# Kernel optimization log

Hardware: AMD Instinct MI355X
Metric: run time of the kernel (lower is better)

The kernel has to match this reference:

```python
import jax, jax.numpy as jnp
import numpy as np

B, N, E, D, H, HW, L = 16, 32, 256, 256, 8, 784, 4
DH = D // H
FF = 4 * D
BN = B * N
BE = B * E
SCALE = 1.0 / np.sqrt(DH)


def _ln(x, g, b):
    m = x.mean(-1, keepdims=True)
    v = ((x - m) ** 2).mean(-1, keepdims=True)
    return (x - m) * jax.lax.rsqrt(v + 1e-5) * g + b


def setup_inputs() -> dict:
    key = jax.random.key(0)
    ks = iter(jax.random.split(key, 64))
    def w(shape, s=0.05):
        return jax.random.normal(next(ks), shape, jnp.float32) * s
    inp = {
        'nodes': w((B, N, D), 1.0),
        'edges': w((B, E, D), 1.0),
        'images': w((B, HW, D), 1.0),
        'mask': jnp.zeros((B * H, N + E, HW), jnp.float32),
        'node_enc': w((BN, D), 1.0),
        'edge_enc': w((BE, D), 1.0),
        'ln1_g': jnp.ones((L, D), jnp.float32), 'ln1_b': jnp.zeros((L, D), jnp.float32),
        'Wqkv': w((L, D, 3 * D)), 'bqkv': jnp.zeros((L, 3 * D), jnp.float32),
        'Wo': w((L, D, D)), 'bo': jnp.zeros((L, D), jnp.float32),
        'ls1': jnp.full((L, D), 0.1, jnp.float32),
        'ln2_g': jnp.ones((L, D), jnp.float32), 'ln2_b': jnp.zeros((L, D), jnp.float32),
        'Wn1': w((L, D, D)), 'bn1': jnp.zeros((L, D), jnp.float32),
        'Wn2': w((L, D, D)), 'bn2': jnp.zeros((L, D), jnp.float32),
        'We': w((L, D, D)), 'be': jnp.zeros((L, D), jnp.float32),
        'attn_p': w((L, H, DH), 1.0),
        'Weo': w((L, D, D)), 'beo': jnp.zeros((L, D), jnp.float32),
        'Wno': w((L, D, D)), 'bno': jnp.zeros((L, D), jnp.float32),
        'ls2': jnp.full((L, D), 0.1, jnp.float32),
        'ln3_g': jnp.ones((L, D), jnp.float32), 'ln3_b': jnp.zeros((L, D), jnp.float32),
        'W1': w((L, D, FF)), 'b1': jnp.zeros((L, FF), jnp.float32),
        'W2': w((L, FF, D)), 'b2': jnp.zeros((L, D), jnp.float32),
        'ls3': jnp.full((L, D), 0.1, jnp.float32),
        'edge_index': jax.random.randint(next(ks), (2, BE), 0, BN, jnp.int32),
    }
    return inp


def reference(nodes, edges, images, mask, node_enc, edge_enc,
              ln1_g, ln1_b, Wqkv, bqkv, Wo, bo, ls1,
              ln2_g, ln2_b, Wn1, bn1, Wn2, bn2, We, be, attn_p, Weo, beo, Wno, bno, ls2,
              ln3_g, ln3_b, W1, b1, W2, b2, ls3, edge_index):
    idx0, idx1 = edge_index[0], edge_index[1]
    ne = jnp.concatenate([nodes, edges], axis=1)  # [B, N+E, D]
    mask4 = mask.reshape(B, H, N + E, HW)
    for l in range(L):
        # cross-attention ne -> images
        ne1n = _ln(ne, ln1_g[l], ln1_b[l])
        q = (ne1n @ Wqkv[l, :, :D] + bqkv[l, :D]).reshape(B, N + E, H, DH)
        k = (images @ Wqkv[l, :, D:2 * D] + bqkv[l, D:2 * D]).reshape(B, HW, H, DH)
        v = (images @ Wqkv[l, :, 2 * D:] + bqkv[l, 2 * D:]).reshape(B, HW, H, DH)
        scores = jnp.einsum('bqhd,bkhd->bhqk', q, k) * SCALE + mask4
        attn = jax.nn.softmax(scores, axis=-1)
        ctx = jnp.einsum('bhqk,bkhd->bqhd', attn, v).reshape(B, N + E, D)
        ne1 = ne + ls1[l] * (ctx @ Wo[l] + bo[l])
        # modified GAT on flattened graph
        ne2n = _ln(ne1, ln2_g[l], ln2_b[l])
        nodes_f = ne2n[:, :N].reshape(BN, D) + node_enc
        edges_f = ne2n[:, N:].reshape(BE, D) + edge_enc
        fn = (nodes_f @ Wn1[l] + bn1[l])[idx0]
        sn = (nodes_f @ Wn2[l] + bn2[l])[idx0]  # NOTE: original code uses edge_index[0] here too
        ep = edges_f @ We[l] + be[l]
        hidden = jax.nn.gelu(fn + sn + ep, approximate=False)  # [BE, D]
        pres = (hidden.reshape(BE, H, DH) * attn_p[l]).sum(-1)  # [BE, H]
        mseg = jax.ops.segment_max(pres, idx0, num_segments=BN)
        expv = jnp.exp(pres - mseg[idx0])
        denom = jax.ops.segment_sum(expv, idx0, num_segments=BN)
        alpha = expv / denom[idx0]  # scatter_softmax over destination nodes
        new_edges = hidden @ Weo[l] + beo[l]
        vals = (nodes_f[idx1] + new_edges) @ Wno[l] + bno[l]
        vals = vals.reshape(BE, H, DH) * alpha[..., None]
        new_nodes = jax.ops.segment_sum(vals.reshape(BE, D), idx0, num_segments=BN)
        gat = jnp.concatenate([new_nodes.reshape(B, N, D), new_edges.reshape(B, E, D)], axis=1)
        ne2 = ne1 + ls2[l] * gat
        # FFN
        ne3n = _ln(ne2, ln3_g[l], ln3_b[l])
        ffn = jax.nn.gelu(ne3n @ W1[l] + b1[l], approximate=False) @ W2[l] + b2[l]
        ne = ne2 + ls3[l] * ffn
    return ne
```

## Files before the change

kernel.cpp:

```cpp
#include <hip/hip_runtime.h>
#include <math.h>

static constexpr int B_  = 16;
static constexpr int N_  = 32;
static constexpr int E_  = 256;
static constexpr int D_  = 256;
static constexpr int H_  = 8;
static constexpr int HW_ = 784;
static constexpr int L_  = 4;
static constexpr int DH_ = 32;
static constexpr int FF_ = 1024;
static constexpr int BN_ = 512;
static constexpr int BE_ = 4096;
static constexpr int NE_ = 288;
#define SCALE_ 0.17677669529663687f

static constexpr size_t LAYER_W = 1114112;
static constexpr size_t OFF_Q   = 0;
static constexpr size_t OFF_K   = 65536;
static constexpr size_t OFF_WO  = 196608;
static constexpr size_t OFF_WN1 = 262144;
static constexpr size_t OFF_WE  = 393216;
static constexpr size_t OFF_WEO = 458752;
static constexpr size_t OFF_WNO = 524288;
static constexpr size_t OFF_W1  = 589824;
static constexpr size_t OFF_W2  = 851968;

typedef __attribute__((ext_vector_type(8))) short bf16x8;
typedef __attribute__((ext_vector_type(4))) float f32x4;

__device__ __forceinline__ float gelu_f(float x) {
    return 0.5f * x * (1.0f + erff(x * 0.7071067811865476f));
}

__device__ __forceinline__ unsigned short f2bf(float x) {
    unsigned u = __float_as_uint(x);
    u += 0x7FFFu + ((u >> 16) & 1u);
    return (unsigned short)(u >> 16);
}
__device__ __forceinline__ unsigned pack2bf(float a, float b) {
    return (unsigned)f2bf(a) | ((unsigned)f2bf(b) << 16);
}
__device__ __forceinline__ float bf2f(unsigned short u) {
    return __uint_as_float(((unsigned)u) << 16);
}


__global__ void concat_kernel(const float* __restrict__ nodes, const float* __restrict__ edges,
                              float* __restrict__ ne) {
    int tid = blockIdx.x * 256 + threadIdx.x;
    int d = tid & 255;
    int row = tid >> 8;
    int b = row / NE_, pos = row % NE_;
    float v = (pos < N_) ? nodes[(size_t)(b * N_ + pos) * D_ + d]
                         : edges[(size_t)(b * E_ + (pos - N_)) * D_ + d];
    ne[tid] = v;
}

__global__ void imgcast_kernel(const float* __restrict__ img, unsigned short* __restrict__ out) {
    int tid = blockIdx.x * 256 + threadIdx.x;
    const float* p = img + (size_t)tid * 8;
    float4 a = *(const float4*)(p);
    float4 b = *(const float4*)(p + 4);
    uint4 o = make_uint4(pack2bf(a.x, a.y), pack2bf(a.z, a.w),
                         pack2bf(b.x, b.y), pack2bf(b.z, b.w));
    *(uint4*)&out[(size_t)tid * 8] = o;
}

__device__ __forceinline__ float ln_from_val(float v, int d,
                                             const float* __restrict__ g, const float* __restrict__ bta,
                                             float* sh1, float* sh2) {
    float s = v, s2 = v * v;
    #pragma unroll
    for (int o = 32; o >= 1; o >>= 1) { s += __shfl_down(s, o); s2 += __shfl_down(s2, o); }
    int lane = d & 63, w = d >> 6;
    if (lane == 0) { sh1[w] = s; sh2[w] = s2; }
    __syncthreads();
    if (d == 0) {
        float a = sh1[0] + sh1[1] + sh1[2] + sh1[3];
        float c = sh2[0] + sh2[1] + sh2[2] + sh2[3];
        sh1[0] = a; sh2[0] = c;
    }
    __syncthreads();
    float mean = sh1[0] * (1.0f / D_);
    float var  = sh2[0] * (1.0f / D_) - mean * mean;
    float rstd = rsqrtf(var + 1e-5f);
    return (v - mean) * rstd * g[d] + bta[d];
}

__global__ __launch_bounds__(256) void ln_kernel(const float* __restrict__ x,
                                                 unsigned short* __restrict__ y,
                                                 const float* __restrict__ g,
                                                 const float* __restrict__ bta) {
    __shared__ float sh1[4], sh2[4];
    const int row = blockIdx.x, d = threadIdx.x;
    float v = x[(size_t)row * D_ + d];
    y[(size_t)row * D_ + d] = f2bf(ln_from_val(v, d, g, bta, sh1, sh2));
}

__global__ __launch_bounds__(256) void ln2enc_kernel(const float* __restrict__ x,
                                                     const float* __restrict__ g,
                                                     const float* __restrict__ bta,
                                                     const float* __restrict__ node_enc,
                                                     const float* __restrict__ edge_enc,
                                                     unsigned short* __restrict__ nodes_f,
                                                     unsigned short* __restrict__ edges_f) {
    __shared__ float sh1[4], sh2[4];
    const int row = blockIdx.x, d = threadIdx.x;
    float v = x[(size_t)row * D_ + d];
    float val = ln_from_val(v, d, g, bta, sh1, sh2);
    int b = row / NE_, pos = row % NE_;
    if (pos < N_) {
        int rn = b * N_ + pos;
        nodes_f[(size_t)rn * D_ + d] = f2bf(val + node_enc[(size_t)rn * D_ + d]);
    } else {
        int re = b * E_ + (pos - N_);
        edges_f[(size_t)re * D_ + d] = f2bf(val + edge_enc[(size_t)re * D_ + d]);
    }
}

__global__ __launch_bounds__(256) void gatres_ln_kernel(
    float* __restrict__ ne, const float* __restrict__ new_nodes,
    const float* __restrict__ new_edges, const float* __restrict__ ls2l,
    const float* __restrict__ g, const float* __restrict__ bta,
    unsigned short* __restrict__ lnb) {
    __shared__ float sh1[4], sh2[4];
    const int row = blockIdx.x, d = threadIdx.x;
    int b = row / NE_, pos = row % NE_;
    float gv = (pos < N_) ? new_nodes[(size_t)(b * N_ + pos) * D_ + d]
                          : new_edges[(size_t)(b * E_ + (pos - N_)) * D_ + d];
    float v = ne[(size_t)row * D_ + d] + ls2l[d] * gv;
    ne[(size_t)row * D_ + d] = v;
    lnb[(size_t)row * D_ + d] = f2bf(ln_from_val(v, d, g, bta, sh1, sh2));
}

__global__ __launch_bounds__(256) void wtrans_kernel(
    const float* __restrict__ Wqkv, const float* __restrict__ Wo,
    const float* __restrict__ Wn1,  const float* __restrict__ Wn2,
    const float* __restrict__ We,   const float* __restrict__ Weo,
    const float* __restrict__ Wno,  const float* __restrict__ W1,
    const float* __restrict__ W2,   unsigned short* __restrict__ wT)
{
    const int bid = blockIdx.x;
    const int l = bid / 1088;
    int tl = bid % 1088;
    const float* src; int ld, K, Nn; unsigned short* dst;
    if (tl < 576) {
        int mid = tl >> 6; tl &= 63;
        K = 256; Nn = 256;
        if (mid < 3) {
            src = Wqkv + (size_t)l * 256 * 768 + mid * 256; ld = 768;
            dst = wT + (size_t)l * LAYER_W + (size_t)mid * 65536;
        } else {
            const float* bases[6] = {Wo, Wn1, Wn2, We, Weo, Wno};
            src = bases[mid - 3] + (size_t)l * 65536; ld = 256;
            dst = wT + (size_t)l * LAYER_W + OFF_WO + (size_t)(mid - 3) * 65536;
        }
    } else if (tl < 832) {
        tl -= 576; K = 256; Nn = 1024;
        src = W1 + (size_t)l * 262144; ld = 1024;
        dst = wT + (size_t)l * LAYER_W + OFF_W1;
    } else {
        tl -= 832; K = 1024; Nn = 256;
        src = W2 + (size_t)l * 262144; ld = 256;
        dst = wT + (size_t)l * LAYER_W + OFF_W2;
    }
    const int ntn = Nn >> 5;
    const int k0 = (tl / ntn) << 5, n0 = (tl % ntn) << 5;
    __shared__ float ts[32][33];
    const int t = threadIdx.x;
    const int kl = t >> 5, nl = t & 31;
    #pragma unroll
    for (int rr = 0; rr < 4; ++rr)
        ts[kl + rr * 8][nl] = src[(size_t)(k0 + kl + rr * 8) * ld + n0 + nl];
    __syncthreads();
    const int onl = t >> 3, okl = (t & 7) << 2;
    ushort4 o;
    o.x = f2bf(ts[okl + 0][onl]); o.y = f2bf(ts[okl + 1][onl]);
    o.z = f2bf(ts[okl + 2][onl]); o.w = f2bf(ts[okl + 3][onl]);
    *(ushort4*)&dst[(size_t)(n0 + onl) * K + k0 + okl] = o;
}

template<int MODE, int OUTBF>
__global__ __launch_bounds__(256) void mgemm_kernel(
    const unsigned short* __restrict__ A, int lda,
    const unsigned short* __restrict__ Bt,
    const float* __restrict__ bias,
    const float* __restrict__ bias2,
    const float* __restrict__ res,
    const float* __restrict__ ls,
    void* __restrict__ Cv, int ldc, int K)
{
    __shared__ unsigned short As[64][72];
    __shared__ unsigned short Bs[64][72];
    const int m0 = blockIdx.y * 64, n0 = blockIdx.x * 64;
    const int t = threadIdx.x;
    const int l = t & 63, w = t >> 6;
    const int wr = (w >> 1) * 32, wc = (w & 1) * 32;
    const int srow = t >> 2, skc = (t & 3) * 16;
    const int frow = l & 15, kg = l >> 4;
    f32x4 acc[2][2];
    acc[0][0] = (f32x4){0.f,0.f,0.f,0.f}; acc[0][1] = acc[0][0];
    acc[1][0] = acc[0][0];                acc[1][1] = acc[0][0];
    for (int k0 = 0; k0 < K; k0 += 64) {
        const unsigned short* ap = A + (size_t)(m0 + srow) * lda + k0 + skc;
        uint4 aq0 = *(const uint4*)(ap);
        uint4 aq1 = *(const uint4*)(ap + 8);
        const unsigned short* bp = Bt + (size_t)(n0 + srow) * K + k0 + skc;
        uint4 bq0 = *(const uint4*)(bp);
        uint4 bq1 = *(const uint4*)(bp + 8);
        __syncthreads();
        *(uint4*)&As[srow][skc]     = aq0;
        *(uint4*)&As[srow][skc + 8] = aq1;
        *(uint4*)&Bs[srow][skc]     = bq0;
        *(uint4*)&Bs[srow][skc + 8] = bq1;
        __syncthreads();
        #pragma unroll
        for (int kk = 0; kk < 2; ++kk) {
            bf16x8 af0 = *(const bf16x8*)&As[wr + frow][kk * 32 + kg * 8];
            bf16x8 af1 = *(const bf16x8*)&As[wr + 16 + frow][kk * 32 + kg * 8];
            bf16x8 bf0 = *(const bf16x8*)&Bs[wc + frow][kk * 32 + kg * 8];
            bf16x8 bf1 = *(const bf16x8*)&Bs[wc + 16 + frow][kk * 32 + kg * 8];
            acc[0][0] = __builtin_amdgcn_mfma_f32_16x16x32_bf16(af0, bf0, acc[0][0], 0, 0, 0);
            acc[0][1] = __builtin_amdgcn_mfma_f32_16x16x32_bf16(af0, bf1, acc[0][1], 0, 0, 0);
            acc[1][0] = __builtin_amdgcn_mfma_f32_16x16x32_bf16(af1, bf0, acc[1][0], 0, 0, 0);
            acc[1][1] = __builtin_amdgcn_mfma_f32_16x16x32_bf16(af1, bf1, acc[1][1], 0, 0, 0);
        }
    }
    #pragma unroll
    for (int fr = 0; fr < 2; ++fr) {
        #pragma unroll
        for (int fc = 0; fc < 2; ++fc) {
            int n = n0 + wc + fc * 16 + frow;
            float bv = (bias2 != nullptr && n >= 256) ? bias2[n - 256] : bias[n];
            float lv = (MODE == 2) ? ls[n] : 0.f;
            #pragma unroll
            for (int rg = 0; rg < 4; ++rg) {
                int m = m0 + wr + fr * 16 + kg * 4 + rg;
                float vv = acc[fr][fc][rg] + bv;
                if (MODE == 1) vv = gelu_f(vv);
                if (MODE == 2) vv = res[(size_t)m * ldc + n] + lv * vv;
                if (OUTBF) ((unsigned short*)Cv)[(size_t)m * ldc + n] = f2bf(vv);
                else       ((float*)Cv)[(size_t)m * ldc + n] = vv;
            }
        }
    }
}

__global__ __launch_bounds__(128) void attn_kernel(
    const unsigned short* __restrict__ q, const unsigned short* __restrict__ kv,
    const float* __restrict__ mask, unsigned short* __restrict__ ctx)
{
    const int bid = blockIdx.x;
    const int h = bid & 7;
    const int qt = (bid >> 3) % 9;
    const int b = (bid >> 3) / 9;
    const int q0 = qt * 32;
    const int t = threadIdx.x;
    const int w = t >> 6, l = t & 63;
    const int lr = l & 15, lg = l >> 4;
    constexpr int NC = (HW_ + 63) / 64;

    __shared__ unsigned short Ks[2][64][40];
    __shared__ unsigned short Vs[2][32][72];
    __shared__ unsigned short Pl[2][16][72];
    __shared__ unsigned short Msk[2][32][68];

    bf16x8 qfrag = *(const bf16x8*)(q + ((size_t)(b * NE_ + q0 + w * 16 + lr)) * D_ + h * DH_ + lg * 8);

    const int kkey = t >> 1, kdh = (t & 1) * 16;
    const int vdh = (t & 7) * 4, vk0 = (t >> 3) * 2;
    const int mrow = t >> 2, mcg = (t & 3) * 16;
    const unsigned short* kbase = kv + ((size_t)b * HW_) * 512 + h * DH_;
    const unsigned short* vbase = kv + ((size_t)b * HW_) * 512 + 256 + h * DH_;
    const float* mbase = mask + ((size_t)(b * H_ + h) * NE_ + q0 + mrow) * (size_t)HW_;

    uint4 kq0, kq1;
    ushort4 va[2], vb4[2];
    float mf[16];

    auto issue_kv = [&](int c0) {
        {
            int key = c0 + kkey;
            bool ok = key < HW_;
            const unsigned short* kp = kbase + (size_t)(ok ? key : 0) * 512 + kdh;
            kq0 = *(const uint4*)(kp);
            kq1 = *(const uint4*)(kp + 8);
            if (!ok) { kq0 = make_uint4(0,0,0,0); kq1 = kq0; }
        }
        #pragma unroll
        for (int r = 0; r < 2; ++r) {
            int key = c0 + vk0 + 32 * r;
            bool ok0 = key < HW_, ok1 = (key + 1) < HW_;
            const unsigned short* vp = vbase + (size_t)(ok0 ? key : 0) * 512 + vdh;
            va[r]  = *(const ushort4*)(vp);
            vb4[r] = *(const ushort4*)(vp + (ok1 ? 512 : 0));
            if (!ok0) va[r]  = make_ushort4(0,0,0,0);
            if (!ok1) vb4[r] = make_ushort4(0,0,0,0);
        }
    };
    auto issue_mask = [&](int c0) {
        if (c0 + 64 <= HW_) {
            #pragma unroll
            for (int i = 0; i < 4; ++i) {
                float4 m4 = *(const float4*)(mbase + c0 + mcg + i * 4);
                mf[i * 4 + 0] = m4.x; mf[i * 4 + 1] = m4.y;
                mf[i * 4 + 2] = m4.z; mf[i * 4 + 3] = m4.w;
            }
        } else {
            #pragma unroll
            for (int i = 0; i < 16; ++i) {
                int col = c0 + mcg + i;
                mf[i] = (col < HW_) ? mbase[col] : -1e30f;
            }
        }
    };
    auto write_kv = [&](int bufi) {
        *(uint4*)&Ks[bufi][kkey][kdh]     = kq0;
        *(uint4*)&Ks[bufi][kkey][kdh + 8] = kq1;
        #pragma unroll
        for (int r = 0; r < 2; ++r) {
            const unsigned short* a = (const unsigned short*)&va[r];
            const unsigned short* c = (const unsigned short*)&vb4[r];
            #pragma unroll
            for (int i = 0; i < 4; ++i)
                *(unsigned*)&Vs[bufi][vdh + i][vk0 + 32 * r] = (unsigned)a[i] | ((unsigned)c[i] << 16);
        }
    };
    auto write_mask = [&](int bufi) {
        uint4 p0 = make_uint4(pack2bf(mf[0], mf[1]),  pack2bf(mf[2], mf[3]),
                              pack2bf(mf[4], mf[5]),  pack2bf(mf[6], mf[7]));
        uint4 p1 = make_uint4(pack2bf(mf[8], mf[9]),  pack2bf(mf[10], mf[11]),
                              pack2bf(mf[12], mf[13]), pack2bf(mf[14], mf[15]));
        *(uint4*)&Msk[bufi][mrow][mcg]     = p0;
        *(uint4*)&Msk[bufi][mrow][mcg + 8] = p1;
    };

    f32x4 oacc[2];
    oacc[0] = (f32x4){0.f, 0.f, 0.f, 0.f}; oacc[1] = oacc[0];
    float m_i[4] = {-INFINITY, -INFINITY, -INFINITY, -INFINITY};
    float l_i[4] = {0.f, 0.f, 0.f, 0.f};

    issue_kv(0);
    issue_mask(0);
    write_kv(0);
    write_mask(0);
    __syncthreads();

    for (int c = 0; c < NC; ++c) {
        const int c0 = c * 64;
        const int cb = c & 1, nb = cb ^ 1;
        if (c + 1 < NC) { issue_kv(c0 + 64); issue_mask(c0 + 64); }

        f32x4 sacc[4];
        #pragma unroll
        for (int fc = 0; fc < 4; ++fc) {
            sacc[fc] = (f32x4){0.f, 0.f, 0.f, 0.f};
            bf16x8 kf = *(const bf16x8*)&Ks[cb][fc * 16 + lr][lg * 8];
            sacc[fc] = __builtin_amdgcn_mfma_f32_16x16x32_bf16(qfrag, kf, sacc[fc], 0, 0, 0);
        }
        float s[4][4];
        #pragma unroll
        for (int fc = 0; fc < 4; ++fc)
            #pragma unroll
            for (int rg = 0; rg < 4; ++rg)
                s[fc][rg] = sacc[fc][rg] * SCALE_ + bf2f(Msk[cb][w * 16 + lg * 4 + rg][fc * 16 + lr]);

        float mloc[4];
        #pragma unroll
        for (int rg = 0; rg < 4; ++rg)
            mloc[rg] = fmaxf(fmaxf(s[0][rg], s[1][rg]), fmaxf(s[2][rg], s[3][rg]));
        #pragma unroll
        for (int off = 1; off < 16; off <<= 1)
            #pragma unroll
            for (int rg = 0; rg < 4; ++rg)
                mloc[rg] = fmaxf(mloc[rg], __shfl_xor(mloc[rg], off));
        float scl[4], lloc[4];
        #pragma unroll
        for (int rg = 0; rg < 4; ++rg) {
            float mn = fmaxf(m_i[rg], mloc[rg]);
            scl[rg] = __expf(m_i[rg] - mn);
            m_i[rg] = mn;
        }
        #pragma unroll
        for (int rg = 0; rg < 4; ++rg) {
            float acc = 0.f;
            #pragma unroll
            for (int fc = 0; fc < 4; ++fc) {
                float p = __expf(s[fc][rg] - m_i[rg]);
                s[fc][rg] = p;
                acc += p;
            }
            lloc[rg] = acc;
        }
        #pragma unroll
        for (int off = 1; off < 16; off <<= 1)
            #pragma unroll
            for (int rg = 0; rg < 4; ++rg)
                lloc[rg] += __shfl_xor(lloc[rg], off);
        #pragma unroll
        for (int rg = 0; rg < 4; ++rg) {
            l_i[rg] = l_i[rg] * scl[rg] + lloc[rg];
            oacc[0][rg] *= scl[rg];
            oacc[1][rg] *= scl[rg];
        }

        #pragma unroll
        for (int fc = 0; fc < 4; ++fc)
            #pragma unroll
            for (int rg = 0; rg < 4; ++rg)
                Pl[w][lg * 4 + rg][fc * 16 + lr] = f2bf(s[fc][rg]);
        #pragma unroll
        for (int ks2 = 0; ks2 < 2; ++ks2) {
            bf16x8 pf = *(const bf16x8*)&Pl[w][lr][ks2 * 32 + lg * 8];
            #pragma unroll
            for (int d2 = 0; d2 < 2; ++d2) {
                bf16x8 vf = *(const bf16x8*)&Vs[cb][d2 * 16 + lr][ks2 * 32 + lg * 8];
                oacc[d2] = __builtin_amdgcn_mfma_f32_16x16x32_bf16(pf, vf, oacc[d2], 0, 0, 0);
            }
        }

        if (c + 1 < NC) {
            write_kv(nb);
            write_mask(nb);
            __syncthreads();
        }
    }

    unsigned short* cbase = ctx + ((size_t)(b * NE_ + q0 + w * 16 + lg * 4)) * D_ + h * DH_;
    #pragma unroll
    for (int rg = 0; rg < 4; ++rg) {
        float inv = 1.0f / l_i[rg];
        #pragma unroll
        for (int d2 = 0; d2 < 2; ++d2)
            cbase[(size_t)rg * D_ + d2 * 16 + lr] = f2bf(oacc[d2][rg] * inv);
    }
}


__global__ __launch_bounds__(256) void hidden_kernel(
    const float* __restrict__ gn12,
    unsigned short* __restrict__ hid, const int* __restrict__ idx0,
    const float* __restrict__ attn_p_l, float* __restrict__ pres) {
    int e = blockIdx.x;
    int d = threadIdx.x;
    int n = idx0[e];
    float x = bf2f(hid[(size_t)e * D_ + d]) + gn12[(size_t)n * 512 + d] + gn12[(size_t)n * 512 + 256 + d];
    float hv = gelu_f(x);
    hid[(size_t)e * D_ + d] = f2bf(hv);
    float pr = hv * attn_p_l[d];
    #pragma unroll
    for (int o = 1; o < 32; o <<= 1) pr += __shfl_xor(pr, o);
    if ((d & 31) == 0) pres[e * H_ + (d >> 5)] = pr;
}

__global__ void segsoft_kernel(const float* __restrict__ pres, const int* __restrict__ csr_off,
                               const int* __restrict__ csr_perm,
                               float* __restrict__ mseg, float* __restrict__ denom) {
    int tid = blockIdx.x * 256 + threadIdx.x;
    int n = tid >> 3, h = tid & 7;
    int s = csr_off[n], e2 = csr_off[n + 1];
    float mx = -INFINITY;
    for (int i = s; i < e2; ++i) mx = fmaxf(mx, pres[csr_perm[i] * H_ + h]);
    float sum = 0.f;
    for (int i = s; i < e2; ++i) sum += expf(pres[csr_perm[i] * H_ + h] - mx);
    mseg[tid] = mx;
    denom[tid] = sum;
}

__global__ void vin_kernel(const unsigned short* __restrict__ nodes_f,
                           const float* __restrict__ new_edges,
                           const int* __restrict__ idx1, unsigned short* __restrict__ vin) {
    int tid = blockIdx.x * 256 + threadIdx.x;
    int e = tid >> 8, d = tid & 255;
    vin[tid] = f2bf(bf2f(nodes_f[(size_t)idx1[e] * D_ + d]) + new_edges[tid]);
}

__global__ __launch_bounds__(256) void nodeagg_kernel(
    const float* __restrict__ vals, const float* __restrict__ pres,
    const float* __restrict__ mseg, const float* __restrict__ denom,
    const int* __restrict__ csr_off, const int* __restrict__ csr_perm,
    float* __restrict__ new_nodes) {
    int n = blockIdx.x;
    int d = threadIdx.x;
    int s = csr_off[n], e2 = csr_off[n + 1];
    int h = d >> 5;
    float ms = mseg[n * H_ + h];
    float rd = 1.0f / denom[n * H_ + h];
    float acc = 0.f;
    for (int i = s; i < e2; ++i) {
        int e = csr_perm[i];
        float a = expf(pres[e * H_ + h] - ms) * rd;
        acc += vals[(size_t)e * D_ + d] * a;
    }
    new_nodes[(size_t)n * D_ + d] = acc;
}


__global__ void zero_counts(int* counts) {
    int t = blockIdx.x * 256 + threadIdx.x;
    if (t < BN_) counts[t] = 0;
}

__global__ void csr_count(const int* __restrict__ idx0, int* __restrict__ counts) {
    int e = blockIdx.x * 256 + threadIdx.x;
    if (e < BE_) atomicAdd(&counts[idx0[e]], 1);
}

__global__ __launch_bounds__(512) void csr_scan(const int* __restrict__ counts, int* __restrict__ csr_off) {
    __shared__ int buf[BN_];
    int t = threadIdx.x;
    int c = counts[t];
    buf[t] = c;
    __syncthreads();
    for (int o = 1; o < BN_; o <<= 1) {
        int add = (t >= o) ? buf[t - o] : 0;
        __syncthreads();
        buf[t] += add;
        __syncthreads();
    }
    csr_off[t] = buf[t] - c;
    if (t == BN_ - 1) csr_off[BN_] = buf[t];
}

__global__ __launch_bounds__(64) void csr_fill(const int* __restrict__ idx0,
                                               const int* __restrict__ csr_off,
                                               int* __restrict__ csr_perm) {
    int n = blockIdx.x;
    int lane = threadIdx.x;
    int w = csr_off[n];
    for (int c0 = 0; c0 < BE_; c0 += 64) {
        int e = c0 + lane;
        bool m = (idx0[e] == n);
        unsigned long long bal = __ballot(m);
        if (m) {
            int pre = __popcll(bal & ((1ull << lane) - 1ull));
            csr_perm[w + pre] = e;
        }
        w += __popcll(bal);
    }
}


static void launch_mgemm(hipStream_t s, int mode, int outbf,
                         const unsigned short* A, int lda, const unsigned short* Bt,
                         const float* bias, const float* bias2, const float* res, const float* ls,
                         void* C, int ldc, int M, int N, int K) {
    dim3 g(N / 64, M / 64);
    if (mode == 0) {
        if (outbf) mgemm_kernel<0,1><<<g, 256, 0, s>>>(A, lda, Bt, bias, bias2, res, ls, C, ldc, K);
        else       mgemm_kernel<0,0><<<g, 256, 0, s>>>(A, lda, Bt, bias, bias2, res, ls, C, ldc, K);
    } else if (mode == 1) {
        mgemm_kernel<1,1><<<g, 256, 0, s>>>(A, lda, Bt, bias, bias2, res, ls, C, ldc, K);
    } else {
        mgemm_kernel<2,0><<<g, 256, 0, s>>>(A, lda, Bt, bias, bias2, res, ls, C, ldc, K);
    }
}

extern "C" void kernel_launch(void* const* d_in, const int* in_sizes, int n_in,
                              void* d_out, int out_size, void* d_ws, size_t ws_size,
                              hipStream_t stream) {
    const float* nodes    = (const float*)d_in[0];
    const float* edges    = (const float*)d_in[1];
    const float* images   = (const float*)d_in[2];
    const float* mask     = (const float*)d_in[3];
    const float* node_enc = (const float*)d_in[4];
    const float* edge_enc = (const float*)d_in[5];
    const float* ln1_g = (const float*)d_in[6];
    const float* ln1_b = (const float*)d_in[7];
    const float* Wqkv  = (const float*)d_in[8];
    const float* bqkv  = (const float*)d_in[9];
    const float* Wo    = (const float*)d_in[10];
    const float* bo    = (const float*)d_in[11];
    const float* ls1   = (const float*)d_in[12];
    const float* ln2_g = (const float*)d_in[13];
    const float* ln2_b = (const float*)d_in[14];
    const float* Wn1   = (const float*)d_in[15];
    const float* bn1   = (const float*)d_in[16];
    const float* Wn2   = (const float*)d_in[17];
    const float* bn2   = (const float*)d_in[18];
    const float* We    = (const float*)d_in[19];
    const float* be    = (const float*)d_in[20];
    const float* attn_p= (const float*)d_in[21];
    const float* Weo   = (const float*)d_in[22];
    const float* beo   = (const float*)d_in[23];
    const float* Wno   = (const float*)d_in[24];
    const float* bno   = (const float*)d_in[25];
    const float* ls2   = (const float*)d_in[26];
    const float* ln3_g = (const float*)d_in[27];
    const float* ln3_b = (const float*)d_in[28];
    const float* W1    = (const float*)d_in[29];
    const float* b1    = (const float*)d_in[30];
    const float* W2    = (const float*)d_in[31];
    const float* b2    = (const float*)d_in[32];
    const float* ls3   = (const float*)d_in[33];
    const int*   edge_index = (const int*)d_in[34];
    const int* idx0 = edge_index;
    const int* idx1 = edge_index + BE_;

    float* ne = (float*)d_out;

    float* cur = (float*)d_ws;
    auto alloc = [&](size_t nfl) { float* p = cur; cur += nfl; return p; };
    auto allocbf = [&](size_t nbf) { float* p = cur; cur += (nbf + 1) / 2; return (unsigned short*)p; };

    unsigned short* lnbuf   = allocbf((size_t)B_ * NE_ * D_);
    unsigned short* qb      = allocbf((size_t)B_ * NE_ * D_);
    unsigned short* kvb     = allocbf((size_t)B_ * HW_ * 512);
    unsigned short* ffnh    = kvb;
    unsigned short* imgbf   = allocbf((size_t)B_ * HW_ * D_);
    unsigned short* ctxb    = allocbf((size_t)B_ * NE_ * D_);
    unsigned short* nodes_f = allocbf((size_t)BN_ * D_);
    unsigned short* edges_f = allocbf((size_t)BE_ * D_);
    unsigned short* hid     = allocbf((size_t)BE_ * D_);
    unsigned short* vin     = allocbf((size_t)BE_ * D_);
    float* gn12     = alloc((size_t)BN_ * 512);
    float* pres     = alloc((size_t)BE_ * H_);
    float* mseg     = alloc((size_t)BN_ * H_);
    float* denom    = alloc((size_t)BN_ * H_);
    float* new_edges= alloc((size_t)BE_ * D_);
    float* valsb    = alloc((size_t)BE_ * D_);
    float* new_nodes= alloc((size_t)BN_ * D_);
    int* counts   = (int*)cur; cur += BN_;
    int* csr_off  = (int*)cur; cur += BN_ + 4;
    int* csr_perm = (int*)cur; cur += BE_;
    cur = (float*)(((uintptr_t)cur + 255) & ~(uintptr_t)255);
    unsigned short* wT = (unsigned short*)cur;

    wtrans_kernel<<<4 * 1088, 256, 0, stream>>>(Wqkv, Wo, Wn1, Wn2, We, Weo, Wno, W1, W2, wT);
    imgcast_kernel<<<(B_ * HW_ * D_) / (256 * 8), 256, 0, stream>>>(images, imgbf);
    zero_counts<<<2, 256, 0, stream>>>(counts);
    csr_count<<<BE_ / 256, 256, 0, stream>>>(idx0, counts);
    csr_scan<<<1, 512, 0, stream>>>(counts, csr_off);
    csr_fill<<<BN_, 64, 0, stream>>>(idx0, csr_off, csr_perm);
    concat_kernel<<<(B_ * NE_ * D_) / 256, 256, 0, stream>>>(nodes, edges, ne);

    for (int l = 0; l < L_; ++l) {
        const unsigned short* wTl = wT + (size_t)l * LAYER_W;
        const float* bqkv_l = bqkv + (size_t)l * 3 * D_;

        ln_kernel<<<B_ * NE_, 256, 0, stream>>>(ne, lnbuf, ln1_g + l * D_, ln1_b + l * D_);
        launch_mgemm(stream, 0, 1, lnbuf, D_, wTl + OFF_Q, bqkv_l, nullptr, nullptr, nullptr,
                     qb, D_, B_ * NE_, D_, D_);
        launch_mgemm(stream, 0, 1, imgbf, D_, wTl + OFF_K, bqkv_l + D_, nullptr, nullptr, nullptr,
                     kvb, 512, B_ * HW_, 512, D_);
        attn_kernel<<<1152, 128, 0, stream>>>(qb, kvb, mask, ctxb);
        launch_mgemm(stream, 2, 0, ctxb, D_, wTl + OFF_WO, bo + l * D_, nullptr, ne, ls1 + l * D_,
                     ne, D_, B_ * NE_, D_, D_);

        ln2enc_kernel<<<B_ * NE_, 256, 0, stream>>>(ne, ln2_g + l * D_, ln2_b + l * D_,
                                                    node_enc, edge_enc, nodes_f, edges_f);
        launch_mgemm(stream, 0, 0, nodes_f, D_, wTl + OFF_WN1, bn1 + l * D_, bn2 + l * D_,
                     nullptr, nullptr, gn12, 512, BN_, 512, D_);
        launch_mgemm(stream, 0, 1, edges_f, D_, wTl + OFF_WE, be + l * D_, nullptr, nullptr, nullptr,
                     hid, D_, BE_, D_, D_);
        hidden_kernel<<<BE_, 256, 0, stream>>>(gn12, hid, idx0, attn_p + (size_t)l * H_ * DH_, pres);
        segsoft_kernel<<<(BN_ * H_) / 256, 256, 0, stream>>>(pres, csr_off, csr_perm, mseg, denom);
        launch_mgemm(stream, 0, 0, hid, D_, wTl + OFF_WEO, beo + l * D_, nullptr, nullptr, nullptr,
                     new_edges, D_, BE_, D_, D_);
        vin_kernel<<<(BE_ * D_) / 256, 256, 0, stream>>>(nodes_f, new_edges, idx1, vin);
        launch_mgemm(stream, 0, 0, vin, D_, wTl + OFF_WNO, bno + l * D_, nullptr, nullptr, nullptr,
                     valsb, D_, BE_, D_, D_);
        nodeagg_kernel<<<BN_, 256, 0, stream>>>(valsb, pres, mseg, denom, csr_off, csr_perm, new_nodes);
        gatres_ln_kernel<<<B_ * NE_, 256, 0, stream>>>(ne, new_nodes, new_edges, ls2 + l * D_,
                                                       ln3_g + l * D_, ln3_b + l * D_, lnbuf);

        launch_mgemm(stream, 1, 1, lnbuf, D_, wTl + OFF_W1, b1 + l * FF_, nullptr, nullptr, nullptr,
                     ffnh, FF_, B_ * NE_, FF_, D_);
        launch_mgemm(stream, 2, 0, ffnh, FF_, wTl + OFF_W2, b2 + l * D_, nullptr, ne, ls3 + l * D_,
                     ne, D_, B_ * NE_, D_, FF_);
    }
}
```

Baseline: 675.8 us.

## Split attention over key halves with combine pass; use direct-to-LDS loads in GEMM

Result: slower. 704.4 us (+4.2%).

```diff
diff --git a/kernel.cpp b/kernel.cpp
--- a/kernel.cpp
+++ b/kernel.cpp
@@ -13,6 +13,7 @@
 static constexpr int BN_ = 512;
 static constexpr int BE_ = 4096;
 static constexpr int NE_ = 288;
+static constexpr int ROWS_ = B_ * H_ * NE_;
 #define SCALE_ 0.17677669529663687f
 
 static constexpr size_t LAYER_W = 1114112;
@@ -28,6 +29,13 @@
 
 typedef __attribute__((ext_vector_type(8))) short bf16x8;
 typedef __attribute__((ext_vector_type(4))) float f32x4;
+
+typedef __attribute__((address_space(1))) const unsigned int gas_uint;
+typedef __attribute__((address_space(3))) unsigned int las_uint;
+
+__device__ __forceinline__ void gload16(const unsigned short* g, unsigned short* lds) {
+    __builtin_amdgcn_global_load_lds((gas_uint*)g, (las_uint*)lds, 16, 0, 0);
+}
 
 __device__ __forceinline__ float gelu_f(float x) {
     return 0.5f * x * (1.0f + erff(x * 0.7071067811865476f));
@@ -191,41 +199,41 @@
     const float* __restrict__ ls,
     void* __restrict__ Cv, int ldc, int K)
 {
-    __shared__ unsigned short As[64][72];
-    __shared__ unsigned short Bs[64][72];
+    __shared__ __align__(16) unsigned short As[64 * 64];
+    __shared__ __align__(16) unsigned short Bs[64 * 64];
     const int m0 = blockIdx.y * 64, n0 = blockIdx.x * 64;
     const int t = threadIdx.x;
     const int l = t & 63, w = t >> 6;
     const int wr = (w >> 1) * 32, wc = (w & 1) * 32;
-    const int srow = t >> 2, skc = (t & 3) * 16;
     const int frow = l & 15, kg = l >> 4;
+    const int srow = w * 8 + (l >> 3);
+    const int scolh = 8 * ((l & 7) ^ (l >> 3));
+    const int ldsoff = w * 512;
+    const int sw = (frow & 7) << 3;
     f32x4 acc[2][2];
     acc[0][0] = (f32x4){0.f,0.f,0.f,0.f}; acc[0][1] = acc[0][0];
     acc[1][0] = acc[0][0];                acc[1][1] = acc[0][0];
     for (int k0 = 0; k0 < K; k0 += 64) {
-        const unsigned short* ap = A + (size_t)(m0 + srow) * lda + k0 + skc;
-        uint4 aq0 = *(const uint4*)(ap);
-        uint4 aq1 = *(const uint4*)(ap + 8);
-        const unsigned short* bp = Bt + (size_t)(n0 + srow) * K + k0 + skc;
-        uint4 bq0 = *(const uint4*)(bp);
-        uint4 bq1 = *(const uint4*)(bp + 8);
+        const unsigned short* ga = A  + (size_t)(m0 + srow) * lda + k0 + scolh;
+        const unsigned short* gb = Bt + (size_t)(n0 + srow) * K   + k0 + scolh;
+        gload16(ga,                As + ldsoff);
+        gload16(ga + 32 * lda,     As + ldsoff + 2048);
+        gload16(gb,                Bs + ldsoff);
+        gload16(gb + (size_t)32 * K, Bs + ldsoff + 2048);
         __syncthreads();
-        *(uint4*)&As[srow][skc]     = aq0;
-        *(uint4*)&As[srow][skc + 8] = aq1;
-        *(uint4*)&Bs[srow][skc]     = bq0;
-        *(uint4*)&Bs[srow][skc + 8] = bq1;
-        __syncthreads();
         #pragma unroll
         for (int kk = 0; kk < 2; ++kk) {
-            bf16x8 af0 = *(const bf16x8*)&As[wr + frow][kk * 32 + kg * 8];
-            bf16x8 af1 = *(const bf16x8*)&As[wr + 16 + frow][kk * 32 + kg * 8];
-            bf16x8 bf0 = *(const bf16x8*)&Bs[wc + frow][kk * 32 + kg * 8];
-            bf16x8 bf1 = *(const bf16x8*)&Bs[wc + 16 + frow][kk * 32 + kg * 8];
+            const int off = (kk * 32 + kg * 8) ^ sw;
+            bf16x8 af0 = *(const bf16x8*)&As[(wr + frow) * 64 + off];
+            bf16x8 af1 = *(const bf16x8*)&As[(wr + 16 + frow) * 64 + off];
+            bf16x8 bf0 = *(const bf16x8*)&Bs[(wc + frow) * 64 + off];
+            bf16x8 bf1 = *(const bf16x8*)&Bs[(wc + 16 + frow) * 64 + off];
             acc[0][0] = __builtin_amdgcn_mfma_f32_16x16x32_bf16(af0, bf0, acc[0][0], 0, 0, 0);
             acc[0][1] = __builtin_amdgcn_mfma_f32_16x16x32_bf16(af0, bf1, acc[0][1], 0, 0, 0);
             acc[1][0] = __builtin_amdgcn_mfma_f32_16x16x32_bf16(af1, bf0, acc[1][0], 0, 0, 0);
             acc[1][1] = __builtin_amdgcn_mfma_f32_16x16x32_bf16(af1, bf1, acc[1][1], 0, 0, 0);
         }
+        __syncthreads();
     }
     #pragma unroll
     for (int fr = 0; fr < 2; ++fr) {
@@ -247,37 +255,38 @@
     }
 }
 
-__global__ __launch_bounds__(128) void attn_kernel(
+__global__ __launch_bounds__(128) void attn_part_kernel(
     const unsigned short* __restrict__ q, const unsigned short* __restrict__ kv,
-    const float* __restrict__ mask, unsigned short* __restrict__ ctx)
+    const float* __restrict__ mask,
+    float* __restrict__ pm, float* __restrict__ pl, float* __restrict__ pO)
 {
     const int bid = blockIdx.x;
-    const int h = bid & 7;
-    const int qt = (bid >> 3) % 9;
-    const int b = (bid >> 3) / 9;
+    const int half = bid & 1;
+    const int h = (bid >> 1) & 7;
+    const int qt = (bid >> 4) % 9;
+    const int b = (bid >> 4) / 9;
     const int q0 = qt * 32;
     const int t = threadIdx.x;
     const int w = t >> 6, l = t & 63;
     const int lr = l & 15, lg = l >> 4;
-    constexpr int NC = (HW_ + 63) / 64;
+    const int cs = half ? 6 : 0;
+    const int nc = half ? 7 : 6;
 
     __shared__ unsigned short Ks[2][64][40];
     __shared__ unsigned short Vs[2][32][72];
     __shared__ unsigned short Pl[2][16][72];
-    __shared__ unsigned short Msk[2][32][68];
 
     bf16x8 qfrag = *(const bf16x8*)(q + ((size_t)(b * NE_ + q0 + w * 16 + lr)) * D_ + h * DH_ + lg * 8);
 
     const int kkey = t >> 1, kdh = (t & 1) * 16;
     const int vdh = (t & 7) * 4, vk0 = (t >> 3) * 2;
-    const int mrow = t >> 2, mcg = (t & 3) * 16;
     const unsigned short* kbase = kv + ((size_t)b * HW_) * 512 + h * DH_;
     const unsigned short* vbase = kv + ((size_t)b * HW_) * 512 + 256 + h * DH_;
-    const float* mbase = mask + ((size_t)(b * H_ + h) * NE_ + q0 + mrow) * (size_t)HW_;
+    const float* mbase = mask + ((size_t)(b * H_ + h) * NE_ + q0 + w * 16 + lg * 4) * (size_t)HW_;
 
     uint4 kq0, kq1;
     ushort4 va[2], vb4[2];
-    float mf[16];
+    float mreg[2][4][4];
 
     auto issue_kv = [&](int c0) {
         {
@@ -299,22 +308,6 @@
             if (!ok1) vb4[r] = make_ushort4(0,0,0,0);
         }
     };
-    auto issue_mask = [&](int c0) {
-        if (c0 + 64 <= HW_) {
-            #pragma unroll
-            for (int i = 0; i < 4; ++i) {
-                float4 m4 = *(const float4*)(mbase + c0 + mcg + i * 4);
-                mf[i * 4 + 0] = m4.x; mf[i * 4 + 1] = m4.y;
-                mf[i * 4 + 2] = m4.z; mf[i * 4 + 3] = m4.w;
-            }
-        } else {
-            #pragma unroll
-            for (int i = 0; i < 16; ++i) {
-                int col = c0 + mcg + i;
-                mf[i] = (col < HW_) ? mbase[col] : -1e30f;
-            }
-        }
-    };
     auto write_kv = [&](int bufi) {
         *(uint4*)&Ks[bufi][kkey][kdh]     = kq0;
         *(uint4*)&Ks[bufi][kkey][kdh + 8] = kq1;
@@ -327,13 +320,14 @@
                 *(unsigned*)&Vs[bufi][vdh + i][vk0 + 32 * r] = (unsigned)a[i] | ((unsigned)c[i] << 16);
         }
     };
-    auto write_mask = [&](int bufi) {
-        uint4 p0 = make_uint4(pack2bf(mf[0], mf[1]),  pack2bf(mf[2], mf[3]),
-                              pack2bf(mf[4], mf[5]),  pack2bf(mf[6], mf[7]));
-        uint4 p1 = make_uint4(pack2bf(mf[8], mf[9]),  pack2bf(mf[10], mf[11]),
-                              pack2bf(mf[12], mf[13]), pack2bf(mf[14], mf[15]));
-        *(uint4*)&Msk[bufi][mrow][mcg]     = p0;
-        *(uint4*)&Msk[bufi][mrow][mcg + 8] = p1;
+    auto issue_mask = [&](int c0, int set) {
+        #pragma unroll
+        for (int rg = 0; rg < 4; ++rg)
+            #pragma unroll
+            for (int fc = 0; fc < 4; ++fc) {
+                int col = c0 + fc * 16 + lr;
+                mreg[set][rg][fc] = (col < HW_) ? mbase[(size_t)rg * HW_ + col] : -1e30f;
+            }
     };
 
     f32x4 oacc[2];
@@ -341,16 +335,17 @@
     float m_i[4] = {-INFINITY, -INFINITY, -INFINITY, -INFINITY};
     float l_i[4] = {0.f, 0.f, 0.f, 0.f};
 
-    issue_kv(0);
-    issue_mask(0);
+    issue_kv(cs * 64);
+    issue_mask(cs * 64, 0);
     write_kv(0);
-    write_mask(0);
+    if (nc > 1) issue_mask(cs * 64 + 64, 1);
     __syncthreads();
 
-    for (int c = 0; c < NC; ++c) {
-        const int c0 = c * 64;
-        const int cb = c & 1, nb = cb ^ 1;
-        if (c + 1 < NC) { issue_kv(c0 + 64); issue_mask(c0 + 64); }
+    for (int i = 0; i < nc; ++i) {
+        const int c0 = (cs + i) * 64;
+        const int cb = i & 1, nb = cb ^ 1;
+        const int set = i & 1;
+        if (i + 1 < nc) issue_kv(c0 + 64);
 
         f32x4 sacc[4];
         #pragma unroll
@@ -364,7 +359,8 @@
         for (int fc = 0; fc < 4; ++fc)
             #pragma unroll
             for (int rg = 0; rg < 4; ++rg)
-                s[fc][rg] = sacc[fc][rg] * SCALE_ + bf2f(Msk[cb][w * 16 + lg * 4 + rg][fc * 16 + lr]);
+                s[fc][rg] = sacc[fc][rg] * SCALE_ + mreg[set][rg][fc];
+        if (i + 2 < nc) issue_mask(c0 + 128, set);
 
         float mloc[4];
         #pragma unroll
@@ -420,21 +416,38 @@
             }
         }
 
-        if (c + 1 < NC) {
+        if (i + 1 < nc) {
             write_kv(nb);
-            write_mask(nb);
             __syncthreads();
         }
     }
 
-    unsigned short* cbase = ctx + ((size_t)(b * NE_ + q0 + w * 16 + lg * 4)) * D_ + h * DH_;
+    const int rowbase = (b * H_ + h) * NE_ + q0 + w * 16 + lg * 4;
     #pragma unroll
     for (int rg = 0; rg < 4; ++rg) {
-        float inv = 1.0f / l_i[rg];
+        size_t gr = (size_t)half * ROWS_ + rowbase + rg;
         #pragma unroll
         for (int d2 = 0; d2 < 2; ++d2)
-            cbase[(size_t)rg * D_ + d2 * 16 + lr] = f2bf(oacc[d2][rg] * inv);
-    }
+            pO[gr * 32 + d2 * 16 + lr] = oacc[d2][rg];
+        if (lr == 0) { pm[gr] = m_i[rg]; pl[gr] = l_i[rg]; }
+    }
+}
+
+__global__ __launch_bounds__(256) void attn_combine_kernel(
+    const float* __restrict__ pm, const float* __restrict__ pl,
+    const float* __restrict__ pO, unsigned short* __restrict__ ctx)
+{
+    int tid = blockIdx.x * 256 + threadIdx.x;
+    int row = tid >> 5, dh = tid & 31;
+    float m0 = pm[row], m1 = pm[ROWS_ + row];
+    float l0 = pl[row], l1 = pl[ROWS_ + row];
+    float mm = fmaxf(m0, m1);
+    float w0 = __expf(m0 - mm), w1 = __expf(m1 - mm);
+    float L = l0 * w0 + l1 * w1;
+    float o = (pO[(size_t)row * 32 + dh] * w0 + pO[((size_t)ROWS_ + row) * 32 + dh] * w1) / L;
+    int bh = row / NE_, qq = row % NE_;
+    int b = bh >> 3, h = bh & 7;
+    ctx[((size_t)(b * NE_ + qq)) * D_ + h * DH_ + dh] = f2bf(o);
 }
 
 
@@ -621,6 +634,9 @@
     float* new_edges= alloc((size_t)BE_ * D_);
     float* valsb    = alloc((size_t)BE_ * D_);
     float* new_nodes= alloc((size_t)BN_ * D_);
+    float* pm       = alloc((size_t)2 * ROWS_);
+    float* pl       = alloc((size_t)2 * ROWS_);
+    float* pO       = alloc((size_t)2 * ROWS_ * 32);
     int* counts   = (int*)cur; cur += BN_;
     int* csr_off  = (int*)cur; cur += BN_ + 4;
     int* csr_perm = (int*)cur; cur += BE_;
@@ -644,7 +660,8 @@
                      qb, D_, B_ * NE_, D_, D_);
         launch_mgemm(stream, 0, 1, imgbf, D_, wTl + OFF_K, bqkv_l + D_, nullptr, nullptr, nullptr,
                      kvb, 512, B_ * HW_, 512, D_);
-        attn_kernel<<<1152, 128, 0, stream>>>(qb, kvb, mask, ctxb);
+        attn_part_kernel<<<2304, 128, 0, stream>>>(qb, kvb, mask, pm, pl, pO);
+        attn_combine_kernel<<<(ROWS_ * 32) / 256, 256, 0, stream>>>(pm, pl, pO, ctxb);
         launch_mgemm(stream, 2, 0, ctxb, D_, wTl + OFF_WO, bo + l * D_, nullptr, ne, ls1 + l * D_,
                      ne, D_, B_ * NE_, D_, D_);
 
```
